# Optimization experiments

Measured on AMD Instinct MI355X. Metric: run time of the kernel, lower is better.

The kernel has to match this reference:

```python
import jax, jax.numpy as jnp
import numpy as np

B, T, C = 2, 1024, 1024
H, N = 16, 64
VOCAB = 32000
W_RANK, A_RANK, V_RANK, G_RANK = 64, 64, 32, 128
EPS_GN = 0.00064


def _wkv(r, w, k, v, a, b):
    # RWKV-7 per-token state recurrence. All args [B,T,C]; per-head state [N,N].
    Bq, Tq, Cq = r.shape
    def rs(u):
        return u.reshape(Bq, Tq, H, N).transpose(1, 0, 2, 3)  # [T,B,H,N]
    r_, k_, v_, a_, b_ = map(rs, (r, k, v, a, b))
    w_ = rs(jnp.exp(-jnp.exp(w.astype(jnp.float32))))  # decay in (0,1)
    def step(S, inp):
        rt, wt, kt, vt, at, bt = inp
        sa = jnp.einsum('bhij,bhj->bhi', S, at)
        S = S * wt[:, :, None, :] + jnp.einsum('bhi,bhj->bhij', sa, bt) + jnp.einsum('bhi,bhj->bhij', vt, kt)
        return S, jnp.einsum('bhij,bhj->bhi', S, rt)
    S0 = jnp.zeros((Bq, H, N, N), jnp.float32)
    _, out = jax.lax.scan(step, S0, (r_, w_, k_, v_, a_, b_))
    return out.transpose(1, 0, 2, 3).reshape(Bq, Tq, Cq).astype(r.dtype)


def _group_norm(x, weight, bias):
    # GroupNorm(H groups, C channels) over [B*T, C], eps=0.00064
    BT, Cq = x.shape
    xg = x.reshape(BT, H, Cq // H)
    mu = xg.mean(-1, keepdims=True)
    var = ((xg - mu) ** 2).mean(-1, keepdims=True)
    xn = ((xg - mu) / jnp.sqrt(var + EPS_GN)).reshape(BT, Cq)
    return xn * weight + bias


def setup_inputs() -> dict:
    key = jax.random.key(0)
    ks = iter(jax.random.split(key, 64))
    def nrm(shape, std):
        return jax.random.normal(next(ks), shape, jnp.float32) * std
    def xav(din, dout):
        return jax.random.normal(next(ks), (din, dout), jnp.float32) * np.float32(np.sqrt(2.0 / (din + dout)))
    inp = {}
    inp['x'] = jax.random.normal(next(ks), (B, T, C), jnp.float32)
    inp['rosa_ids'] = jax.random.randint(next(ks), (B, T), 0, VOCAB)
    for nm in ['x_r', 'x_w', 'x_k', 'x_v', 'x_a', 'x_g']:
        inp[nm] = nrm((1, 1, C), 0.01)
    for nm in ['w0', 'a0', 'v0']:
        inp[nm] = nrm((1, 1, C), 0.02)
    inp['w1'] = xav(C, W_RANK); inp['w2'] = xav(W_RANK, C)
    inp['a1'] = xav(C, A_RANK); inp['a2'] = xav(A_RANK, C)
    inp['v1'] = xav(C, V_RANK); inp['v2'] = xav(V_RANK, C)
    inp['g1'] = xav(C, G_RANK); inp['g2'] = xav(G_RANK, C)
    inp['k_k'] = 1.0 + nrm((1, 1, C), 0.02)
    inp['k_a'] = nrm((1, 1, C), 0.02)
    inp['r_k'] = nrm((H, N), 0.01)
    inp['Wr'] = xav(C, C); inp['Wk'] = xav(C, C); inp['Wv'] = xav(C, C); inp['Wo'] = xav(C, C)
    inp['ln_w'] = jnp.ones((C,), jnp.float32)
    inp['ln_b'] = jnp.zeros((C,), jnp.float32)
    inp['rosa_emb'] = nrm((VOCAB, C), 0.02)
    inp['rosa_gate'] = nrm((1, 1, C), 0.01)
    return inp


def reference(x, rosa_ids, x_r, x_w, x_k, x_v, x_a, x_g, w0, a0, v0,
              w1, w2, a1, a2, v1, v2, g1, g2, k_k, k_a, r_k,
              Wr, Wk, Wv, Wo, ln_w, ln_b, rosa_emb, rosa_gate):
    Bq, Tq, Cq = x.shape
    # time_shift: shift tokens right by one, zero-pad front
    xx = jnp.concatenate([jnp.zeros((Bq, 1, Cq), x.dtype), x[:, :-1]], axis=1) - x
    xr, xw, xk, xv, xa, xg = (x + xx * m for m in (x_r, x_w, x_k, x_v, x_a, x_g))
    r = xr @ Wr
    w = w0 + jnp.tanh(xw @ w1) @ w2
    k = xk @ Wk
    v = xv @ Wv
    # first-call v_first behavior: v_first = v.detach()
    v_first = jax.lax.stop_gradient(v)
    v = v + (v_first - v) * jax.nn.sigmoid(v0 + (xv @ v1) @ v2)
    a = jax.nn.sigmoid(a0 + (xa @ a1) @ a2)
    g = jax.nn.sigmoid(xg @ g1) @ g2
    kk = (k * k_k).reshape(Bq, Tq, H, N)
    kk = kk / jnp.maximum(jnp.linalg.norm(kk, axis=-1, keepdims=True), 1e-12)
    kk = kk.reshape(Bq, Tq, Cq)
    k = k * (1.0 + (a - 1.0) * k_a)
    o = _wkv(r, w, k, v, -kk, kk * a)
    o = _group_norm(o.reshape(Bq * Tq, Cq), ln_w, ln_b).reshape(Bq, Tq, Cq)
    rkv = ((r.reshape(Bq, Tq, H, N) * k.reshape(Bq, Tq, H, N) * r_k).sum(-1, keepdims=True)
           * v.reshape(Bq, Tq, H, N)).reshape(Bq, Tq, Cq)
    o = o + rkv
    emb = rosa_emb[rosa_ids]
    gate = jax.nn.sigmoid(o * rosa_gate).mean(-1, keepdims=True)
    o = o * (1.0 - gate) + emb * gate
    return (o * g) @ Wo
```

## Files before the change

### kernel.cpp

```cpp
#include <hip/hip_runtime.h>
#include <hip/hip_bf16.h>
#include <hip/hip_fp16.h>
#include <math.h>

constexpr int Bb = 2, Tt = 1024, Cc = 1024, Hh = 16, Nn = 64;
constexpr int Mtot = Bb * Tt;
constexpr int PACKW = 6 * Nn;
constexpr int SL_R = 0, SL_W = 1, SL_K = 2, SL_V = 3, SL_NK = 4, SL_BV = 5;

typedef _Float16 half8 __attribute__((ext_vector_type(8)));
typedef float f32x4 __attribute__((ext_vector_type(4)));

__device__ __forceinline__ float sigf(float x) { return 1.f / (1.f + expf(-x)); }

__device__ __forceinline__ unsigned short f2h(float f) {
    _Float16 h = (_Float16)f;
    return __builtin_bit_cast(unsigned short, h);
}

__global__ __launch_bounds__(256) void mixcast_k(
    const float* __restrict__ x, const float* __restrict__ mr,
    const float* __restrict__ mk, const float* __restrict__ mv,
    const float* __restrict__ mw, const float* __restrict__ ma,
    const float* __restrict__ mg, unsigned short* __restrict__ xf)
{
    int idx = (blockIdx.x * 256 + threadIdx.x) * 4;
    int m = idx >> 10, c = idx & 1023;
    int t = m & (Tt - 1);
    float4 xc = *(const float4*)(x + idx);
    float4 xp = make_float4(0.f, 0.f, 0.f, 0.f);
    if (t) xp = *(const float4*)(x + idx - Cc);
    float4 d = make_float4(xp.x - xc.x, xp.y - xc.y, xp.z - xc.z, xp.w - xc.w);
    float4 m4;
    ushort4 o4;
#define EMIT(mixp, zoff)                                               \
    m4 = *(const float4*)(mixp + c);                                   \
    o4.x = f2h(xc.x + d.x * m4.x); o4.y = f2h(xc.y + d.y * m4.y);      \
    o4.z = f2h(xc.z + d.z * m4.z); o4.w = f2h(xc.w + d.w * m4.w);      \
    *(ushort4*)(xf + (size_t)(zoff)*2097152 + idx) = o4;
    EMIT(mr, 0)
    EMIT(mk, 1)
    EMIT(mv, 2)
    EMIT(mw, 3)
    EMIT(ma, 4)
    EMIT(mg, 5)
#undef EMIT
}

__global__ __launch_bounds__(256) void wtrans_k(
    const float* __restrict__ W0, const float* __restrict__ W1,
    const float* __restrict__ W2, const float* __restrict__ W3,
    unsigned short* __restrict__ WT)
{
    __shared__ float ls[64][65];
    const int z = blockIdx.z;
    const float* W = (z == 0) ? W0 : (z == 1) ? W1 : (z == 2) ? W2 : W3;
    unsigned short* dst = WT + (size_t)z * Cc * Cc;
    const int k0 = blockIdx.x * 64, n0 = blockIdx.y * 64;
    const int tid = threadIdx.x;
    const int rr = tid >> 4, c4 = tid & 15;
#pragma unroll
    for (int q = 0; q < 4; q++) {
        int kr = rr + q * 16;
        float4 v = *(const float4*)(W + (size_t)(k0 + kr) * Cc + n0 + c4 * 4);
        ls[kr][c4 * 4 + 0] = v.x; ls[kr][c4 * 4 + 1] = v.y;
        ls[kr][c4 * 4 + 2] = v.z; ls[kr][c4 * 4 + 3] = v.w;
    }
    __syncthreads();
#pragma unroll
    for (int q = 0; q < 4; q++) {
        int nr = rr + q * 16;
        ushort4 o;
        o.x = f2h(ls[c4 * 4 + 0][nr]);
        o.y = f2h(ls[c4 * 4 + 1][nr]);
        o.z = f2h(ls[c4 * 4 + 2][nr]);
        o.w = f2h(ls[c4 * 4 + 3][nr]);
        *(ushort4*)(dst + (size_t)(n0 + nr) * Cc + k0 + c4 * 4) = o;
    }
}

__global__ __launch_bounds__(256) void tr6_k(
    const float* __restrict__ w1, const float* __restrict__ a1, const float* __restrict__ g1,
    const float* __restrict__ w2, const float* __restrict__ a2, const float* __restrict__ g2,
    unsigned short* __restrict__ wts)
{
    int t = blockIdx.x;
    const float* src; unsigned short* dst; int R, C, tr, tc;
    if (t < 16)      { src = w1; dst = wts + 0;      R = 1024; C = 64;   tr = t;            tc = 0; }
    else if (t < 32) { src = a1; dst = wts + 65536;  R = 1024; C = 64;   tr = t - 16;       tc = 0; }
    else if (t < 64) { src = g1; dst = wts + 131072; R = 1024; C = 128;  tr = (t - 32) >> 1; tc = (t - 32) & 1; }
    else if (t < 80) { src = w2; dst = wts + 262144; R = 64;   C = 1024; tr = 0;            tc = t - 64; }
    else if (t < 96) { src = a2; dst = wts + 327680; R = 64;   C = 1024; tr = 0;            tc = t - 80; }
    else             { src = g2; dst = wts + 393216; R = 128;  C = 1024; tr = (t - 96) & 1; tc = (t - 96) >> 1; }
    __shared__ float ls[64][65];
    const int tid = threadIdx.x, rr = tid >> 4, c4 = tid & 15;
    const int r0 = tr * 64, c0 = tc * 64;
#pragma unroll
    for (int q = 0; q < 4; q++) {
        int r = rr + q * 16;
        float4 v = *(const float4*)(src + (size_t)(r0 + r) * C + c0 + c4 * 4);
        ls[r][c4 * 4 + 0] = v.x; ls[r][c4 * 4 + 1] = v.y;
        ls[r][c4 * 4 + 2] = v.z; ls[r][c4 * 4 + 3] = v.w;
    }
    __syncthreads();
#pragma unroll
    for (int q = 0; q < 4; q++) {
        int c = rr + q * 16;
        ushort4 o;
        o.x = f2h(ls[c4 * 4 + 0][c]);
        o.y = f2h(ls[c4 * 4 + 1][c]);
        o.z = f2h(ls[c4 * 4 + 2][c]);
        o.w = f2h(ls[c4 * 4 + 3][c]);
        *(ushort4*)(dst + (size_t)(c0 + c) * R + r0 + c4 * 4) = o;
    }
}

template <int RKV>
__global__ __launch_bounds__(256) void mgemm_k(
    const unsigned short* __restrict__ Abase, const unsigned short* __restrict__ WT,
    float* __restrict__ out, int M, int Ncol, int K)
{
    __shared__ unsigned short Ash[2][128][40];
    __shared__ unsigned short Bsh[2][64][40];
    const int z = RKV ? blockIdx.z : 0;
    const unsigned short* A = Abase + (size_t)z * 2097152;
    const unsigned short* BT = WT + (size_t)z * 1048576;
    const int tid = threadIdx.x;
    const int lane = tid & 63, wid = tid >> 6;
    const int wr = wid >> 1, wc = wid & 1;
    const int bm = blockIdx.y * 128, bn = blockIdx.x * 64;
    const int l15 = lane & 15, lk = lane >> 4;
    const int srow = tid >> 2, skc = tid & 3;

    f32x4 acc[4][2];
#pragma unroll
    for (int i = 0; i < 4; i++)
#pragma unroll
        for (int j = 0; j < 2; j++) acc[i][j] = (f32x4){0.f, 0.f, 0.f, 0.f};

    uint4 ra0, ra1, rb0;
    const size_t arow = (size_t)(bm + srow) * K + skc * 8;
    const size_t brow = (size_t)(bn + srow) * K + skc * 8;

#define LOADG(k0)                                                  \
    ra0 = *(const uint4*)(A + arow + (k0));                        \
    ra1 = *(const uint4*)(A + arow + (size_t)64 * K + (k0));       \
    rb0 = *(const uint4*)(BT + brow + (k0));
#define WRITEL(buf)                                                \
    *(uint4*)&Ash[buf][srow][skc * 8] = ra0;                       \
    *(uint4*)&Ash[buf][srow + 64][skc * 8] = ra1;                  \
    *(uint4*)&Bsh[buf][srow][skc * 8] = rb0;

    LOADG(0)
    WRITEL(0)
    __syncthreads();

    int cur = 0;
    for (int k0 = 0; k0 < K; k0 += 32) {
        const bool pf = (k0 + 32 < K);
        if (pf) { LOADG(k0 + 32) }
        half8 af[4], bf[2];
#pragma unroll
        for (int m = 0; m < 4; m++)
            af[m] = *(const half8*)&Ash[cur][wr * 64 + m * 16 + l15][lk * 8];
#pragma unroll
        for (int n = 0; n < 2; n++)
            bf[n] = *(const half8*)&Bsh[cur][wc * 32 + n * 16 + l15][lk * 8];
#pragma unroll
        for (int m = 0; m < 4; m++)
#pragma unroll
            for (int n = 0; n < 2; n++)
                acc[m][n] = __builtin_amdgcn_mfma_f32_16x16x32_f16(af[m], bf[n], acc[m][n], 0, 0, 0);
        if (pf) { WRITEL(cur ^ 1) }
        __syncthreads();
        cur ^= 1;
    }
#undef LOADG
#undef WRITEL

    const int slot = (z == 0) ? SL_R : (z == 1) ? SL_K : SL_V;
#pragma unroll
    for (int m = 0; m < 4; m++) {
#pragma unroll
        for (int n = 0; n < 2; n++) {
            int col = bn + wc * 32 + n * 16 + l15;
#pragma unroll
            for (int r = 0; r < 4; r++) {
                int row = bm + wr * 64 + m * 16 + lk * 4 + r;
                float cval = acc[m][n][r];
                if (RKV == 0) {
                    out[(size_t)row * Ncol + col] = cval;
                } else {
                    int b = row >> 10, t = row & (Tt - 1);
                    int h = col >> 6, nn2 = col & 63;
                    out[((size_t)(b * Hh + h) * Tt + t) * PACKW + slot * Nn + nn2] = cval;
                }
            }
        }
    }
}

__global__ __launch_bounds__(256) void lr1_k(
    const unsigned short* __restrict__ xf, const unsigned short* __restrict__ wts,
    unsigned short* __restrict__ h1)
{
    __shared__ unsigned short Ash[2][128][40];
    __shared__ unsigned short Bsh[2][64][40];
    const int bx = blockIdx.x;
    const unsigned short* A = xf + (size_t)(bx == 0 ? 3 : bx == 1 ? 4 : 5) * 2097152;
    const unsigned short* BT = wts + (bx == 0 ? 0 : bx == 1 ? 65536 : 131072 + (bx - 2) * 65536);
    const int colbase = bx * 64;
    const int K = 1024;
    const int tid = threadIdx.x;
    const int lane = tid & 63, wid = tid >> 6;
    const int wr = wid >> 1, wc = wid & 1;
    const int bm = blockIdx.y * 128;
    const int l15 = lane & 15, lk = lane >> 4;
    const int srow = tid >> 2, skc = tid & 3;

    f32x4 acc[4][2];
#pragma unroll
    for (int i = 0; i < 4; i++)
#pragma unroll
        for (int j = 0; j < 2; j++) acc[i][j] = (f32x4){0.f, 0.f, 0.f, 0.f};

    uint4 ra0, ra1, rb0;
    const size_t arow = (size_t)(bm + srow) * K + skc * 8;
    const size_t brow = (size_t)srow * K + skc * 8;

#define LOADG(k0)                                                  \
    ra0 = *(const uint4*)(A + arow + (k0));                        \
    ra1 = *(const uint4*)(A + arow + (size_t)64 * K + (k0));       \
    rb0 = *(const uint4*)(BT + brow + (k0));
#define WRITEL(buf)                                                \
    *(uint4*)&Ash[buf][srow][skc * 8] = ra0;                       \
    *(uint4*)&Ash[buf][srow + 64][skc * 8] = ra1;                  \
    *(uint4*)&Bsh[buf][srow][skc * 8] = rb0;

    LOADG(0)
    WRITEL(0)
    __syncthreads();

    int cur = 0;
    for (int k0 = 0; k0 < K; k0 += 32) {
        const bool pf = (k0 + 32 < K);
        if (pf) { LOADG(k0 + 32) }
        half8 af[4], bf[2];
#pragma unroll
        for (int m = 0; m < 4; m++)
            af[m] = *(const half8*)&Ash[cur][wr * 64 + m * 16 + l15][lk * 8];
#pragma unroll
        for (int n = 0; n < 2; n++)
            bf[n] = *(const half8*)&Bsh[cur][wc * 32 + n * 16 + l15][lk * 8];
#pragma unroll
        for (int m = 0; m < 4; m++)
#pragma unroll
            for (int n = 0; n < 2; n++)
                acc[m][n] = __builtin_amdgcn_mfma_f32_16x16x32_f16(af[m], bf[n], acc[m][n], 0, 0, 0);
        if (pf) { WRITEL(cur ^ 1) }
        __syncthreads();
        cur ^= 1;
    }
#undef LOADG
#undef WRITEL

#pragma unroll
    for (int m = 0; m < 4; m++) {
#pragma unroll
        for (int n = 0; n < 2; n++) {
            int col = colbase + wc * 32 + n * 16 + l15;
#pragma unroll
            for (int r = 0; r < 4; r++) {
                int row = bm + wr * 64 + m * 16 + lk * 4 + r;
                float c = acc[m][n][r];
                if (bx == 0) c = tanhf(c);
                else if (bx >= 2) c = sigf(c);
                h1[(size_t)row * 256 + col] = f2h(c);
            }
        }
    }
}

__global__ __launch_bounds__(256) void lr2_k(
    const unsigned short* __restrict__ h1, const unsigned short* __restrict__ wts,
    const float* __restrict__ w0, const float* __restrict__ a0,
    float* __restrict__ pack, float* __restrict__ gbuf)
{
    __shared__ unsigned short Ash[128][40];
    __shared__ unsigned short Bsh[64][40];
    const int z = blockIdx.z;
    const int K = (z == 2) ? 128 : 64;
    const int aoff = (z == 0) ? 0 : (z == 1) ? 64 : 128;
    const unsigned short* BT = wts + 262144 + z * 65536;
    const int tid = threadIdx.x;
    const int lane = tid & 63, wid = tid >> 6;
    const int wr = wid >> 1, wc = wid & 1;
    const int bm = blockIdx.y * 128, bn = blockIdx.x * 64;
    const int l15 = lane & 15, lk = lane >> 4;
    const int srow = tid >> 2, skc = tid & 3;

    f32x4 acc[4][2];
#pragma unroll
    for (int i = 0; i < 4; i++)
#pragma unroll
        for (int j = 0; j < 2; j++) acc[i][j] = (f32x4){0.f, 0.f, 0.f, 0.f};

    for (int k0 = 0; k0 < K; k0 += 32) {
        uint4 ra0 = *(const uint4*)(h1 + (size_t)(bm + srow) * 256 + aoff + k0 + skc * 8);
        uint4 ra1 = *(const uint4*)(h1 + (size_t)(bm + srow + 64) * 256 + aoff + k0 + skc * 8);
        uint4 rb0 = *(const uint4*)(BT + (size_t)(bn + srow) * K + k0 + skc * 8);
        *(uint4*)&Ash[srow][skc * 8] = ra0;
        *(uint4*)&Ash[srow + 64][skc * 8] = ra1;
        *(uint4*)&Bsh[srow][skc * 8] = rb0;
        __syncthreads();
        half8 af[4], bf[2];
#pragma unroll
        for (int m = 0; m < 4; m++)
            af[m] = *(const half8*)&Ash[wr * 64 + m * 16 + l15][lk * 8];
#pragma unroll
        for (int n = 0; n < 2; n++)
            bf[n] = *(const half8*)&Bsh[wc * 32 + n * 16 + l15][lk * 8];
#pragma unroll
        for (int m = 0; m < 4; m++)
#pragma unroll
            for (int n = 0; n < 2; n++)
                acc[m][n] = __builtin_amdgcn_mfma_f32_16x16x32_f16(af[m], bf[n], acc[m][n], 0, 0, 0);
        __syncthreads();
    }

#pragma unroll
    for (int m = 0; m < 4; m++) {
#pragma unroll
        for (int n = 0; n < 2; n++) {
            int col = bn + wc * 32 + n * 16 + l15;
#pragma unroll
            for (int r = 0; r < 4; r++) {
                int row = bm + wr * 64 + m * 16 + lk * 4 + r;
                float c = acc[m][n][r];
                int b = row >> 10, t = row & (Tt - 1);
                int h = col >> 6, nn2 = col & 63;
                if (z == 0) {
                    pack[((size_t)(b * Hh + h) * Tt + t) * PACKW + SL_W * Nn + nn2] = expf(-expf(w0[col] + c));
                } else if (z == 1) {
                    pack[((size_t)(b * Hh + h) * Tt + t) * PACKW + SL_BV * Nn + nn2] = sigf(a0[col] + c);
                } else {
                    gbuf[(size_t)row * Cc + col] = c;
                }
            }
        }
    }
}

__global__ __launch_bounds__(256) void prep_k(float* __restrict__ pk,
                                              const float* __restrict__ k_k,
                                              const float* __restrict__ k_a)
{
    int inst = blockIdx.x * 4 + (threadIdx.x >> 6);
    int lane = threadIdx.x & 63;
    int b = inst >> 14;
    int rem = inst & 16383;
    int t = rem >> 4;
    int h = rem & 15;
    size_t base = ((size_t)(b * Hh + h) * Tt + t) * PACKW;
    int c = h * 64 + lane;
    float kraw = pk[base + SL_K * 64 + lane];
    float a = pk[base + SL_BV * 64 + lane];
    float kkv = kraw * k_k[c];
    float ss = kkv * kkv;
#pragma unroll
    for (int m = 1; m < 64; m <<= 1) ss += __shfl_xor(ss, m);
    float kkn = kkv / fmaxf(sqrtf(ss), 1e-12f);
    pk[base + SL_NK * 64 + lane] = -kkn;
    pk[base + SL_BV * 64 + lane] = kkn * a;
    pk[base + SL_K * 64 + lane] = kraw * (1.f + (a - 1.f) * k_a[c]);
}

template <int C>
__device__ __forceinline__ float dppmov(float x) {
    return __int_as_float(__builtin_amdgcn_mov_dpp(__float_as_int(x), C, 0xF, 0xF, 1));
}
__device__ __forceinline__ float red16(float v) {
    v += dppmov<0xB1>(v);
    v += dppmov<0x4E>(v);
    v += dppmov<0x141>(v);
    v += dppmov<0x140>(v);
    return v;
}

struct Slot { f32x4 r, w, k, n, b; float v; };

__device__ __forceinline__ void stepf6(f32x4& S, const Slot& f, int jb, float* optr)
{
    float sa = fmaf(S[3], f.n[3], fmaf(S[2], f.n[2], fmaf(S[1], f.n[1], S[0] * f.n[0])));
    sa = red16(sa);
    S[0] = fmaf(S[0], f.w[0], fmaf(sa, f.b[0], f.v * f.k[0]));
    S[1] = fmaf(S[1], f.w[1], fmaf(sa, f.b[1], f.v * f.k[1]));
    S[2] = fmaf(S[2], f.w[2], fmaf(sa, f.b[2], f.v * f.k[2]));
    S[3] = fmaf(S[3], f.w[3], fmaf(sa, f.b[3], f.v * f.k[3]));
    float ot = fmaf(S[3], f.r[3], fmaf(S[2], f.r[2], fmaf(S[1], f.r[1], S[0] * f.r[0])));
    ot = red16(ot);
    if (jb == 0) *optr = ot;
}

__global__ __launch_bounds__(64, 1) void wkv_k(const float* __restrict__ pk, float* __restrict__ o)
{
    const int bx = blockIdx.x;
    const int xcd = bx & 7;
    const int ix = bx >> 3;
    const int bh = ((ix >> 4) << 3) | xcd;
    const int rg = ix & 15;
    const int lane = threadIdx.x;
    const int ri = lane >> 4, jb = lane & 15, j0 = jb * 4;
    const int i = rg * 4 + ri;
    const int b = bh >> 4, h = bh & 15;
    const float* pb = pk + (size_t)bh * Tt * PACKW;
    float* ob = o + (size_t)b * Tt * Cc + h * 64 + i;

    Slot sl[8];
    const float* p1 = pb + j0;
    const float* p2 = pb + SL_V * 64 + i;

#define ISSUE(s, q1v, q2v)                                                                                \
    asm volatile("global_load_dwordx4 %0, %1, off"             : "=v"(sl[s].r) : "v"(q1v) : "memory");    \
    asm volatile("global_load_dwordx4 %0, %1, off offset:256"  : "=v"(sl[s].w) : "v"(q1v) : "memory");    \
    asm volatile("global_load_dwordx4 %0, %1, off offset:512"  : "=v"(sl[s].k) : "v"(q1v) : "memory");    \
    asm volatile("global_load_dwordx4 %0, %1, off offset:1024" : "=v"(sl[s].n) : "v"(q1v) : "memory");    \
    asm volatile("global_load_dwordx4 %0, %1, off offset:1280" : "=v"(sl[s].b) : "v"(q1v) : "memory");    \
    asm volatile("global_load_dword %0, %1, off"               : "=v"(sl[s].v) : "v"(q2v) : "memory");

    ISSUE(0, p1 + 0 * PACKW, p2 + 0 * PACKW)
    ISSUE(1, p1 + 1 * PACKW, p2 + 1 * PACKW)
    ISSUE(2, p1 + 2 * PACKW, p2 + 2 * PACKW)
    ISSUE(3, p1 + 3 * PACKW, p2 + 3 * PACKW)
    ISSUE(4, p1 + 4 * PACKW, p2 + 4 * PACKW)
    ISSUE(5, p1 + 5 * PACKW, p2 + 5 * PACKW)
    ISSUE(6, p1 + 6 * PACKW, p2 + 6 * PACKW)
    ISSUE(7, p1 + 7 * PACKW, p2 + 7 * PACKW)

    const float* q1 = p1 + 8 * PACKW;
    const float* q2 = p2 + 8 * PACKW;
    f32x4 S = (f32x4){0.f, 0.f, 0.f, 0.f};

#define STEP(u)                                                          \
    asm volatile("s_waitcnt vmcnt(42)" ::: "memory");                    \
    __builtin_amdgcn_sched_barrier(0);                                   \
    stepf6(S, sl[u], jb, ob + (size_t)(t0 + (u)) * Cc);                  \
    ISSUE(u, q1, q2)                                                     \
    if (t0 + (u) + 9 < Tt) { q1 += PACKW; q2 += PACKW; }

    for (int t0 = 0; t0 < Tt; t0 += 8) {
        STEP(0) STEP(1) STEP(2) STEP(3) STEP(4) STEP(5) STEP(6) STEP(7)
    }
#undef STEP
#undef ISSUE
}

__global__ __launch_bounds__(256) void post_k(
    const float* __restrict__ o, const float* __restrict__ pk, const float* __restrict__ gbuf,
    const float* __restrict__ r_k, const float* __restrict__ ln_w, const float* __restrict__ ln_b,
    const int* __restrict__ ids, const float* __restrict__ emb, const float* __restrict__ rgate,
    unsigned short* __restrict__ outh)
{
    __shared__ float sred[4];
    const int bt = blockIdx.x;
    const int b = bt >> 10, t = bt & 1023;
    const int tid = threadIdx.x;
    const int c0 = tid * 4;
    const int h = tid >> 4;
    const int nn = c0 & 63;

    float4 o4 = *(const float4*)(o + (size_t)bt * Cc + c0);
    float s = o4.x + o4.y + o4.z + o4.w;
    float ss = o4.x * o4.x + o4.y * o4.y + o4.z * o4.z + o4.w * o4.w;
#pragma unroll
    for (int m = 1; m < 16; m <<= 1) { s += __shfl_xor(s, m); ss += __shfl_xor(ss, m); }
    float mu = s * (1.f / 64.f);
    float inv = rsqrtf(ss * (1.f / 64.f) - mu * mu + 0.00064f);

    size_t pbase = ((size_t)(b * Hh + h) * Tt + t) * PACKW;
    float4 r4 = *(const float4*)(pk + pbase + SL_R * 64 + nn);
    float4 k4 = *(const float4*)(pk + pbase + SL_K * 64 + nn);
    float4 v4 = *(const float4*)(pk + pbase + SL_V * 64 + nn);
    float4 q4 = *(const float4*)(r_k + h * 64 + nn);
    float dot = r4.x * k4.x * q4.x + r4.y * k4.y * q4.y + r4.z * k4.z * q4.z + r4.w * k4.w * q4.w;
#pragma unroll
    for (int m = 1; m < 16; m <<= 1) dot += __shfl_xor(dot, m);

    float4 lw = *(const float4*)(ln_w + c0);
    float4 lb = *(const float4*)(ln_b + c0);
    float e0 = (o4.x - mu) * inv * lw.x + lb.x + dot * v4.x;
    float e1 = (o4.y - mu) * inv * lw.y + lb.y + dot * v4.y;
    float e2 = (o4.z - mu) * inv * lw.z + lb.z + dot * v4.z;
    float e3 = (o4.w - mu) * inv * lw.w + lb.w + dot * v4.w;

    float4 rg4 = *(const float4*)(rgate + c0);
    float gp = sigf(e0 * rg4.x) + sigf(e1 * rg4.y) + sigf(e2 * rg4.z) + sigf(e3 * rg4.w);
#pragma unroll
    for (int m = 1; m < 64; m <<= 1) gp += __shfl_xor(gp, m);
    if ((tid & 63) == 0) sred[tid >> 6] = gp;
    __syncthreads();
    float gate = (sred[0] + sred[1] + sred[2] + sred[3]) * (1.f / 1024.f);

    const int id = ids[bt];
    float4 em = *(const float4*)(emb + (size_t)id * Cc + c0);
    float4 g4 = *(const float4*)(gbuf + (size_t)bt * Cc + c0);
    ushort4 h4;
    h4.x = f2h((e0 * (1.f - gate) + em.x * gate) * g4.x);
    h4.y = f2h((e1 * (1.f - gate) + em.y * gate) * g4.y);
    h4.z = f2h((e2 * (1.f - gate) + em.z * gate) * g4.z);
    h4.w = f2h((e3 * (1.f - gate) + em.w * gate) * g4.w);
    *(ushort4*)(outh + (size_t)bt * Cc + c0) = h4;
}

extern "C" void kernel_launch(void* const* d_in, const int* in_sizes, int n_in,
                              void* d_out, int out_size, void* d_ws, size_t ws_size,
                              hipStream_t stream)
{
    (void)in_sizes; (void)n_in; (void)out_size; (void)ws_size;
    const float* x    = (const float*)d_in[0];
    const int*   ids  = (const int*)d_in[1];
    const float* x_r  = (const float*)d_in[2];
    const float* x_w  = (const float*)d_in[3];
    const float* x_k  = (const float*)d_in[4];
    const float* x_v  = (const float*)d_in[5];
    const float* x_a  = (const float*)d_in[6];
    const float* x_g  = (const float*)d_in[7];
    const float* w0   = (const float*)d_in[8];
    const float* a0   = (const float*)d_in[9];
    const float* w1   = (const float*)d_in[11];
    const float* w2   = (const float*)d_in[12];
    const float* a1   = (const float*)d_in[13];
    const float* a2   = (const float*)d_in[14];
    const float* g1   = (const float*)d_in[17];
    const float* g2   = (const float*)d_in[18];
    const float* k_k  = (const float*)d_in[19];
    const float* k_a  = (const float*)d_in[20];
    const float* r_k  = (const float*)d_in[21];
    const float* Wr   = (const float*)d_in[22];
    const float* Wk   = (const float*)d_in[23];
    const float* Wv   = (const float*)d_in[24];
    const float* Wo   = (const float*)d_in[25];
    const float* ln_w = (const float*)d_in[26];
    const float* ln_b = (const float*)d_in[27];
    const float* emb  = (const float*)d_in[28];
    const float* rg   = (const float*)d_in[29];

    float* ws = (float*)d_ws;
    float* pack = ws;
    float* obuf = pack + (size_t)12582912;
    float* gbuf = obuf + (size_t)2097152;
    unsigned short* xf  = (unsigned short*)(gbuf + (size_t)2097152);
    unsigned short* wt  = xf + (size_t)6 * 2097152;
    unsigned short* wts = wt + (size_t)4 * 1048576;
    unsigned short* h1  = wts + (size_t)524288;
    unsigned short* obh = xf;

    dim3 blk(256);

    wtrans_k<<<dim3(16, 16, 4), blk, 0, stream>>>(Wr, Wk, Wv, Wo, wt);
    tr6_k<<<dim3(128), blk, 0, stream>>>(w1, a1, g1, w2, a2, g2, wts);
    mixcast_k<<<dim3(2048), blk, 0, stream>>>(x, x_r, x_k, x_v, x_w, x_a, x_g, xf);

    mgemm_k<1><<<dim3(Cc / 64, Mtot / 128, 3), blk, 0, stream>>>(xf, wt, pack, Mtot, Cc, Cc);
    lr1_k<<<dim3(4, 16), blk, 0, stream>>>(xf, wts, h1);
    lr2_k<<<dim3(16, 16, 3), blk, 0, stream>>>(h1, wts, w0, a0, pack, gbuf);

    prep_k<<<dim3(Bb * Tt * Hh / 4), blk, 0, stream>>>(pack, k_k, k_a);
    wkv_k<<<dim3(512), dim3(64), 0, stream>>>(pack, obuf);
    post_k<<<dim3(Mtot), blk, 0, stream>>>(obuf, pack, gbuf, r_k, ln_w, ln_b, ids, emb, rg, obh);
    mgemm_k<0><<<dim3(Cc / 64, Mtot / 128, 1), blk, 0, stream>>>(obh, wt + (size_t)3 * 1048576, (float*)d_out, Mtot, Cc, Cc);
}
```

Baseline: 233.4 us.

## Pack WKV inputs as fp16 interleaved buffer and split state rows across more waves

```diff
diff --git a/kernel.cpp b/kernel.cpp
--- a/kernel.cpp
+++ b/kernel.cpp
@@ -7,15 +7,23 @@
 constexpr int Mtot = Bb * Tt;
 constexpr int PACKW = 6 * Nn;
 constexpr int SL_R = 0, SL_W = 1, SL_K = 2, SL_V = 3, SL_NK = 4, SL_BV = 5;
+constexpr int PK2S = 768;
 
 typedef _Float16 half8 __attribute__((ext_vector_type(8)));
 typedef float f32x4 __attribute__((ext_vector_type(4)));
+typedef unsigned int u32x4 __attribute__((ext_vector_type(4)));
 
 __device__ __forceinline__ float sigf(float x) { return 1.f / (1.f + expf(-x)); }
 
 __device__ __forceinline__ unsigned short f2h(float f) {
     _Float16 h = (_Float16)f;
     return __builtin_bit_cast(unsigned short, h);
+}
+__device__ __forceinline__ float h2lo(unsigned int u) {
+    return (float)__builtin_bit_cast(_Float16, (unsigned short)(u & 0xffffu));
+}
+__device__ __forceinline__ float h2hi(unsigned int u) {
+    return (float)__builtin_bit_cast(_Float16, (unsigned short)(u >> 16));
 }
 
 __global__ __launch_bounds__(256) void mixcast_k(
@@ -352,6 +360,7 @@
 }
 
 __global__ __launch_bounds__(256) void prep_k(float* __restrict__ pk,
+                                              unsigned char* __restrict__ pk2,
                                               const float* __restrict__ k_k,
                                               const float* __restrict__ k_a)
 {
@@ -363,96 +372,107 @@
     int h = rem & 15;
     size_t base = ((size_t)(b * Hh + h) * Tt + t) * PACKW;
     int c = h * 64 + lane;
+    float rv   = pk[base + SL_R * 64 + lane];
+    float wv   = pk[base + SL_W * 64 + lane];
     float kraw = pk[base + SL_K * 64 + lane];
-    float a = pk[base + SL_BV * 64 + lane];
+    float vv   = pk[base + SL_V * 64 + lane];
+    float a    = pk[base + SL_BV * 64 + lane];
     float kkv = kraw * k_k[c];
     float ss = kkv * kkv;
 #pragma unroll
     for (int m = 1; m < 64; m <<= 1) ss += __shfl_xor(ss, m);
     float kkn = kkv / fmaxf(sqrtf(ss), 1e-12f);
-    pk[base + SL_NK * 64 + lane] = -kkn;
-    pk[base + SL_BV * 64 + lane] = kkn * a;
-    pk[base + SL_K * 64 + lane] = kraw * (1.f + (a - 1.f) * k_a[c]);
+    float kmod = kraw * (1.f + (a - 1.f) * k_a[c]);
+    pk[base + SL_K * 64 + lane] = kmod;
+
+    unsigned char* sb = pk2 + ((size_t)(b * Hh + h) * Tt + t) * PK2S;
+    int p = lane >> 1, hf = lane & 1;
+    unsigned int lo = (unsigned)f2h(rv) | ((unsigned)f2h(kmod) << 16);
+    unsigned int hi = (unsigned)f2h(-kkn) | ((unsigned)f2h(kkn * a) << 16);
+    *(unsigned int*)(sb + p * 16 + hf * 8) = lo;
+    *(unsigned int*)(sb + p * 16 + hf * 8 + 4) = hi;
+    *(unsigned short*)(sb + 512 + lane * 2) = f2h(wv);
+    *(unsigned short*)(sb + 640 + lane * 2) = f2h(vv);
 }
 
 template <int C>
 __device__ __forceinline__ float dppmov(float x) {
     return __int_as_float(__builtin_amdgcn_mov_dpp(__float_as_int(x), C, 0xF, 0xF, 1));
 }
-__device__ __forceinline__ float red16(float v) {
+__device__ __forceinline__ float red32(float v) {
     v += dppmov<0xB1>(v);
     v += dppmov<0x4E>(v);
     v += dppmov<0x141>(v);
     v += dppmov<0x140>(v);
+    v += __shfl_xor(v, 16);
     return v;
 }
 
-struct Slot { f32x4 r, w, k, n, b; float v; };
-
-__device__ __forceinline__ void stepf6(f32x4& S, const Slot& f, int jb, float* optr)
-{
-    float sa = fmaf(S[3], f.n[3], fmaf(S[2], f.n[2], fmaf(S[1], f.n[1], S[0] * f.n[0])));
-    sa = red16(sa);
-    S[0] = fmaf(S[0], f.w[0], fmaf(sa, f.b[0], f.v * f.k[0]));
-    S[1] = fmaf(S[1], f.w[1], fmaf(sa, f.b[1], f.v * f.k[1]));
-    S[2] = fmaf(S[2], f.w[2], fmaf(sa, f.b[2], f.v * f.k[2]));
-    S[3] = fmaf(S[3], f.w[3], fmaf(sa, f.b[3], f.v * f.k[3]));
-    float ot = fmaf(S[3], f.r[3], fmaf(S[2], f.r[2], fmaf(S[1], f.r[1], S[0] * f.r[0])));
-    ot = red16(ot);
+struct Slot { u32x4 d; unsigned int w; unsigned int v; };
+
+__device__ __forceinline__ void stepf7(float& S0, float& S1, const Slot& f, int jb, float* optr)
+{
+    float r0 = h2lo(f.d[0]), k0 = h2hi(f.d[0]);
+    float n0 = h2lo(f.d[1]), b0 = h2hi(f.d[1]);
+    float r1 = h2lo(f.d[2]), k1 = h2hi(f.d[2]);
+    float n1 = h2lo(f.d[3]), b1 = h2hi(f.d[3]);
+    float w0 = h2lo(f.w),  w1 = h2hi(f.w);
+    float vv = h2lo(f.v);
+    float sa = fmaf(S1, n1, S0 * n0);
+    sa = red32(sa);
+    S0 = fmaf(S0, w0, fmaf(sa, b0, vv * k0));
+    S1 = fmaf(S1, w1, fmaf(sa, b1, vv * k1));
+    float ot = fmaf(S1, r1, S0 * r0);
+    ot = red32(ot);
     if (jb == 0) *optr = ot;
 }
 
-__global__ __launch_bounds__(64, 1) void wkv_k(const float* __restrict__ pk, float* __restrict__ o)
+__global__ __launch_bounds__(64, 1) void wkv_k(const unsigned char* __restrict__ pk2,
+                                               float* __restrict__ o)
 {
     const int bx = blockIdx.x;
     const int xcd = bx & 7;
     const int ix = bx >> 3;
-    const int bh = ((ix >> 4) << 3) | xcd;
-    const int rg = ix & 15;
+    const int bh = xcd * 4 + (ix >> 5);
+    const int rg = ix & 31;
     const int lane = threadIdx.x;
-    const int ri = lane >> 4, jb = lane & 15, j0 = jb * 4;
-    const int i = rg * 4 + ri;
+    const int ri = lane >> 5;
+    const int jb = lane & 31;
+    const int row = rg * 2 + ri;
     const int b = bh >> 4, h = bh & 15;
-    const float* pb = pk + (size_t)bh * Tt * PACKW;
-    float* ob = o + (size_t)b * Tt * Cc + h * 64 + i;
+    const unsigned char* base = pk2 + (size_t)bh * Tt * PK2S;
+    const unsigned char* pq = base + jb * 16;
+    const unsigned char* pw = base + 512 + jb * 4;
+    const unsigned char* pv = base + 640 + row * 2;
+    float* ob = o + (size_t)b * Tt * Cc + h * 64 + row;
 
     Slot sl[8];
-    const float* p1 = pb + j0;
-    const float* p2 = pb + SL_V * 64 + i;
-
-#define ISSUE(s, q1v, q2v)                                                                                \
-    asm volatile("global_load_dwordx4 %0, %1, off"             : "=v"(sl[s].r) : "v"(q1v) : "memory");    \
-    asm volatile("global_load_dwordx4 %0, %1, off offset:256"  : "=v"(sl[s].w) : "v"(q1v) : "memory");    \
-    asm volatile("global_load_dwordx4 %0, %1, off offset:512"  : "=v"(sl[s].k) : "v"(q1v) : "memory");    \
-    asm volatile("global_load_dwordx4 %0, %1, off offset:1024" : "=v"(sl[s].n) : "v"(q1v) : "memory");    \
-    asm volatile("global_load_dwordx4 %0, %1, off offset:1280" : "=v"(sl[s].b) : "v"(q1v) : "memory");    \
-    asm volatile("global_load_dword %0, %1, off"               : "=v"(sl[s].v) : "v"(q2v) : "memory");
-
-    ISSUE(0, p1 + 0 * PACKW, p2 + 0 * PACKW)
-    ISSUE(1, p1 + 1 * PACKW, p2 + 1 * PACKW)
-    ISSUE(2, p1 + 2 * PACKW, p2 + 2 * PACKW)
-    ISSUE(3, p1 + 3 * PACKW, p2 + 3 * PACKW)
-    ISSUE(4, p1 + 4 * PACKW, p2 + 4 * PACKW)
-    ISSUE(5, p1 + 5 * PACKW, p2 + 5 * PACKW)
-    ISSUE(6, p1 + 6 * PACKW, p2 + 6 * PACKW)
-    ISSUE(7, p1 + 7 * PACKW, p2 + 7 * PACKW)
-
-    const float* q1 = p1 + 8 * PACKW;
-    const float* q2 = p2 + 8 * PACKW;
-    f32x4 S = (f32x4){0.f, 0.f, 0.f, 0.f};
+
+#define ISSUE(s)                                                                                     \
+    asm volatile("global_load_dwordx4 %0, %1, off" : "=v"(sl[s].d) : "v"(pq) : "memory");            \
+    asm volatile("global_load_dword %0, %1, off"   : "=v"(sl[s].w) : "v"(pw) : "memory");            \
+    asm volatile("global_load_ushort %0, %1, off"  : "=v"(sl[s].v) : "v"(pv) : "memory");
+#define ADV { pq += PK2S; pw += PK2S; pv += PK2S; }
+
+    ISSUE(0) ADV ISSUE(1) ADV ISSUE(2) ADV ISSUE(3) ADV
+    ISSUE(4) ADV ISSUE(5) ADV ISSUE(6) ADV ISSUE(7) ADV
+
+    float S0 = 0.f, S1 = 0.f;
 
 #define STEP(u)                                                          \
-    asm volatile("s_waitcnt vmcnt(42)" ::: "memory");                    \
     __builtin_amdgcn_sched_barrier(0);                                   \
-    stepf6(S, sl[u], jb, ob + (size_t)(t0 + (u)) * Cc);                  \
-    ISSUE(u, q1, q2)                                                     \
-    if (t0 + (u) + 9 < Tt) { q1 += PACKW; q2 += PACKW; }
+    asm volatile("s_waitcnt vmcnt(21)" ::: "memory");                    \
+    __builtin_amdgcn_sched_barrier(0);                                   \
+    stepf7(S0, S1, sl[u], jb, ob + (size_t)(t0 + (u)) * Cc);             \
+    ISSUE(u)                                                             \
+    if (t0 + (u) + 9 < Tt) ADV
 
     for (int t0 = 0; t0 < Tt; t0 += 8) {
         STEP(0) STEP(1) STEP(2) STEP(3) STEP(4) STEP(5) STEP(6) STEP(7)
     }
 #undef STEP
 #undef ISSUE
+#undef ADV
 }
 
 __global__ __launch_bounds__(256) void post_k(
@@ -554,6 +574,7 @@
     unsigned short* wts = wt + (size_t)4 * 1048576;
     unsigned short* h1  = wts + (size_t)524288;
     unsigned short* obh = xf;
+    unsigned char*  pk2 = (unsigned char*)(xf + (size_t)2097152);
 
     dim3 blk(256);
 
@@ -565,8 +586,8 @@
     lr1_k<<<dim3(4, 16), blk, 0, stream>>>(xf, wts, h1);
     lr2_k<<<dim3(16, 16, 3), blk, 0, stream>>>(h1, wts, w0, a0, pack, gbuf);
 
-    prep_k<<<dim3(Bb * Tt * Hh / 4), blk, 0, stream>>>(pack, k_k, k_a);
-    wkv_k<<<dim3(512), dim3(64), 0, stream>>>(pack, obuf);
+    prep_k<<<dim3(Bb * Tt * Hh / 4), blk, 0, stream>>>(pack, pk2, k_k, k_a);
+    wkv_k<<<dim3(1024), dim3(64), 0, stream>>>(pk2, obuf);
     post_k<<<dim3(Mtot), blk, 0, stream>>>(obuf, pack, gbuf, r_k, ln_w, ln_b, ids, emb, rg, obh);
     mgemm_k<0><<<dim3(Cc / 64, Mtot / 128, 1), blk, 0, stream>>>(obh, wt + (size_t)3 * 1048576, (float*)d_out, Mtot, Cc, Cc);
 }
```

Result: slower. 310.3 us (+32.9%).
